# Optimization experiments

Measured on AMD Instinct MI355X. Metric: run time of the kernel, lower is better.

Reference implementation:

```python
import jax, jax.numpy as jnp
import numpy as np

B, S, H, NH = 2, 2048, 1024, 16
HD = H // NH  # 64


def rope_cos_sin(seq_len, dim, base=10000.0, dtype=jnp.float32):
    inv_freq = 1.0 / (base ** (jnp.arange(0, dim, 2, dtype=jnp.float32) / dim))
    t = jnp.arange(seq_len, dtype=jnp.float32)
    freqs = jnp.outer(t, inv_freq)              # [S, dim/2]
    emb = jnp.concatenate([freqs, freqs], -1)   # [S, dim]
    # broadcast shape [1, S, 1, dim]
    return jnp.cos(emb)[None, :, None, :].astype(dtype), jnp.sin(emb)[None, :, None, :].astype(dtype)


def rotate_half(x):
    x1, x2 = x[..., : x.shape[-1] // 2], x[..., x.shape[-1] // 2:]
    return jnp.concatenate([-x2, x1], axis=-1)


def setup_inputs() -> dict:
    key = jax.random.key(0)
    ks = jax.random.split(key, 5)
    sc = 1.0 / np.sqrt(H)
    x = jax.random.normal(ks[0], (B, S, H), jnp.float32)
    Wq = jax.random.normal(ks[1], (H, H), jnp.float32) * sc
    Wk = jax.random.normal(ks[2], (H, H), jnp.float32) * sc
    Wv = jax.random.normal(ks[3], (H, H), jnp.float32) * sc
    Wo = jax.random.normal(ks[4], (H, H), jnp.float32) * sc
    z = jnp.zeros((H,), jnp.float32)
    mask = jnp.tril(jnp.ones((S, S), bool))[None, None]  # causal [1,1,S,S]
    return {"x": x, "Wq": Wq, "bq": z, "Wk": Wk, "bk": z, "Wv": Wv, "bv": z,
            "Wo": Wo, "bo": z, "mask": mask}


def reference(x, Wq, bq, Wk, bk, Wv, bv, Wo, bo, mask):
    b, s, _ = x.shape
    q = (x @ Wq.T + bq).reshape(b, s, NH, HD)
    k = (x @ Wk.T + bk).reshape(b, s, NH, HD)
    v = (x @ Wv.T + bv).reshape(b, s, NH, HD)
    cos, sin = rope_cos_sin(s, HD, dtype=x.dtype)
    q = q * cos + rotate_half(q) * sin
    k = k * cos + rotate_half(k) * sin
    # [b, h, s, s] scores, explicit as in original
    scores = jnp.einsum("bqhd,bkhd->bhqk", q, k) / jnp.sqrt(jnp.asarray(HD, x.dtype))
    scores = jnp.where(mask, scores, jnp.asarray(-jnp.inf, x.dtype))
    attn = jax.nn.softmax(scores, axis=-1)
    out = jnp.einsum("bhqk,bkhd->bqhd", attn, v).reshape(b, s, H)
    return out @ Wo.T + bo
```

## Files before the change

kernel.cpp:

```cpp
#include <hip/hip_runtime.h>

typedef __bf16 bf16;
typedef __bf16 bf16x4 __attribute__((ext_vector_type(4)));
typedef __bf16 bf16x8 __attribute__((ext_vector_type(8)));
typedef float floatx4 __attribute__((ext_vector_type(4)));

#define MFMA16(a, b, c) __builtin_amdgcn_mfma_f32_16x16x32_bf16(a, b, c, 0, 0, 0)

__device__ __forceinline__ void load_lds16(const void* g, void* l) {
    __builtin_amdgcn_global_load_lds(
        (const __attribute__((address_space(1))) unsigned int*)g,
        (__attribute__((address_space(3))) unsigned int*)l, 16, 0, 0);
}

__device__ __forceinline__ bf16x8 scale8(bf16x8 a, float s) {
    bf16x8 o;
    #pragma unroll
    for (int i = 0; i < 8; i++) o[i] = (bf16)((float)a[i] * s);
    return o;
}

__global__ __launch_bounds__(256) void cvt_all_kernel(
    const float* __restrict__ x, const float* __restrict__ wq,
    const float* __restrict__ wk, const float* __restrict__ wv,
    const float* __restrict__ wo,
    bf16* __restrict__ xb, bf16* __restrict__ wqb, bf16* __restrict__ wkb,
    bf16* __restrict__ wvb, bf16* __restrict__ wob)
{
    int bid = blockIdx.x;
    const float* src; bf16* dst; int off;
    if (bid < 4096)      { src = x;  dst = xb;  off = bid; }
    else if (bid < 5120) { src = wq; dst = wqb; off = bid - 4096; }
    else if (bid < 6144) { src = wk; dst = wkb; off = bid - 5120; }
    else if (bid < 7168) { src = wv; dst = wvb; off = bid - 6144; }
    else                 { src = wo; dst = wob; off = bid - 7168; }
    int idx = (off * 256 + threadIdx.x) * 4;
    float4 v = *(const float4*)&src[idx];
    bf16x4 o;
    o[0] = (bf16)v.x; o[1] = (bf16)v.y; o[2] = (bf16)v.z; o[3] = (bf16)v.w;
    *(bf16x4*)&dst[idx] = o;
}

__global__ __launch_bounds__(256) void cvt_kernel(const float* __restrict__ x,
                                                  bf16* __restrict__ xb) {
    int idx = (blockIdx.x * 256 + threadIdx.x) * 4;
    float4 v = *(const float4*)&x[idx];
    bf16x4 o;
    o[0] = (bf16)v.x; o[1] = (bf16)v.y; o[2] = (bf16)v.z; o[3] = (bf16)v.w;
    *(bf16x4*)&xb[idx] = o;
}


#define STAGE_TILES(Asrc, Bsrc, arow, brow)                                   \
    _Pragma("unroll")                                                         \
    for (int t = 0; t < 4; t++) {                                             \
        int R0 = w * 32 + t * 8;                                              \
        int row = R0 + (lane >> 3);                                           \
        int gc = (lane & 7) ^ (row & 7);                                      \
        load_lds16(&Asrc[(size_t)(arow + row) * 1024 + k0 + gc * 8], &As[R0][0]); \
        load_lds16(&Bsrc[(size_t)(brow + row) * 1024 + k0 + gc * 8], &Bs[R0][0]); \
    }

__global__ __launch_bounds__(256) void gemm_qkv_fast(
    const bf16* __restrict__ xb,
    const bf16* __restrict__ Wq, const bf16* __restrict__ Wk,
    const bf16* __restrict__ Wv,
    const float* __restrict__ bq, const float* __restrict__ bk,
    const float* __restrict__ bv,
    bf16* __restrict__ q_ws, bf16* __restrict__ k_ws, bf16* __restrict__ vt_ws)
{
    int m0 = blockIdx.x * 128;
    int n0 = blockIdx.y * 128;
    int sec = n0 >> 10;
    int nw0 = n0 & 1023;
    const bf16* W     = (sec == 0) ? Wq : (sec == 1) ? Wk : Wv;
    const float* bias = (sec == 0) ? bq : (sec == 1) ? bk : bv;

    __shared__ bf16 As[128][64];
    __shared__ bf16 Bs[128][64];

    int tid = threadIdx.x;
    int lane = tid & 63, w = tid >> 6;
    int l15 = lane & 15, quad = lane >> 4;
    int wm = (w >> 1) * 64, wn = (w & 1) * 64;

    floatx4 acc[4][4];
    #pragma unroll
    for (int i = 0; i < 4; i++)
        #pragma unroll
        for (int j = 0; j < 4; j++) acc[i][j] = (floatx4){0.f, 0.f, 0.f, 0.f};

    for (int k0 = 0; k0 < 1024; k0 += 64) {
        __syncthreads();
        STAGE_TILES(xb, W, m0, nw0)
        __syncthreads();
        #pragma unroll
        for (int kk = 0; kk < 2; kk++) {
            int cb = kk * 4 + quad;
            bf16x8 af[4], bfr[4];
            #pragma unroll
            for (int mt = 0; mt < 4; mt++) {
                int row = wm + mt * 16 + l15;
                af[mt] = *(const bf16x8*)&As[row][(cb ^ (row & 7)) * 8];
            }
            #pragma unroll
            for (int nt = 0; nt < 4; nt++) {
                int row = wn + nt * 16 + l15;
                bfr[nt] = *(const bf16x8*)&Bs[row][(cb ^ (row & 7)) * 8];
            }
            #pragma unroll
            for (int mt = 0; mt < 4; mt++)
                #pragma unroll
                for (int nt = 0; nt < 4; nt++)
                    acc[mt][nt] = MFMA16(af[mt], bfr[nt], acc[mt][nt]);
        }
    }

    if (sec < 2) {
        bf16* outp = (sec == 0) ? q_ws : k_ws;
        float inv[2];
        inv[0] = __expf(-(float)l15 * (9.210340371976184f / 32.0f));
        inv[1] = __expf(-(float)(16 + l15) * (9.210340371976184f / 32.0f));
        #pragma unroll
        for (int mt = 0; mt < 4; mt++) {
            #pragma unroll
            for (int r = 0; r < 4; r++) {
                int m = m0 + wm + mt * 16 + quad * 4 + r;
                int bb = m >> 11, s = m & 2047;
                #pragma unroll
                for (int nt = 0; nt < 2; nt++) {
                    int nl1 = nw0 + wn + nt * 16 + l15;
                    int nl2 = nl1 + 32;
                    float x1 = acc[mt][nt][r] + bias[nl1];
                    float x2 = acc[mt][nt + 2][r] + bias[nl2];
                    float ang = (float)s * inv[nt];
                    float sn, cs;
                    __sincosf(ang, &sn, &cs);
                    int hh = nl1 >> 6, d = nl1 & 63;
                    size_t base = ((size_t)(bb * 16 + hh) * 2048 + s) * 64;
                    outp[base + d]      = (bf16)(x1 * cs - x2 * sn);
                    outp[base + d + 32] = (bf16)(x2 * cs + x1 * sn);
                }
            }
        }
    } else {
        #pragma unroll
        for (int mt = 0; mt < 4; mt++) {
            int mbase = m0 + wm + mt * 16 + quad * 4;
            int bb = mbase >> 11, s0 = mbase & 2047;
            #pragma unroll
            for (int nt = 0; nt < 4; nt++) {
                int nl = nw0 + wn + nt * 16 + l15;
                int hh = nl >> 6, d = nl & 63;
                bf16x4 pk;
                #pragma unroll
                for (int r = 0; r < 4; r++) pk[r] = (bf16)(acc[mt][nt][r] + bias[nl]);
                *(bf16x4*)&vt_ws[((size_t)(bb * 16 + hh) * 64 + d) * 2048 + s0] = pk;
            }
        }
    }
}

__global__ __launch_bounds__(256) void gemm_out_fast(
    const bf16* __restrict__ A, const bf16* __restrict__ W,
    const float* __restrict__ bias, float* __restrict__ out)
{
    int m0 = blockIdx.x * 128;
    int n0 = blockIdx.y * 128;

    __shared__ bf16 As[128][64];
    __shared__ bf16 Bs[128][64];

    int tid = threadIdx.x;
    int lane = tid & 63, w = tid >> 6;
    int l15 = lane & 15, quad = lane >> 4;
    int wm = (w >> 1) * 64, wn = (w & 1) * 64;

    floatx4 acc[4][4];
    #pragma unroll
    for (int i = 0; i < 4; i++)
        #pragma unroll
        for (int j = 0; j < 4; j++) acc[i][j] = (floatx4){0.f, 0.f, 0.f, 0.f};

    for (int k0 = 0; k0 < 1024; k0 += 64) {
        __syncthreads();
        STAGE_TILES(A, W, m0, n0)
        __syncthreads();
        #pragma unroll
        for (int kk = 0; kk < 2; kk++) {
            int cb = kk * 4 + quad;
            bf16x8 af[4], bfr[4];
            #pragma unroll
            for (int mt = 0; mt < 4; mt++) {
                int row = wm + mt * 16 + l15;
                af[mt] = *(const bf16x8*)&As[row][(cb ^ (row & 7)) * 8];
            }
            #pragma unroll
            for (int nt = 0; nt < 4; nt++) {
                int row = wn + nt * 16 + l15;
                bfr[nt] = *(const bf16x8*)&Bs[row][(cb ^ (row & 7)) * 8];
            }
            #pragma unroll
            for (int mt = 0; mt < 4; mt++)
                #pragma unroll
                for (int nt = 0; nt < 4; nt++)
                    acc[mt][nt] = MFMA16(af[mt], bfr[nt], acc[mt][nt]);
        }
    }

    #pragma unroll
    for (int mt = 0; mt < 4; mt++) {
        #pragma unroll
        for (int r = 0; r < 4; r++) {
            int m = m0 + wm + mt * 16 + quad * 4 + r;
            #pragma unroll
            for (int nt = 0; nt < 4; nt++) {
                int nl = n0 + wn + nt * 16 + l15;
                out[(size_t)m * 1024 + nl] = acc[mt][nt][r] + bias[nl];
            }
        }
    }
}

__global__ __launch_bounds__(256) void gemm_qkv_f32w(
    const bf16* __restrict__ xb,
    const float* __restrict__ Wq, const float* __restrict__ Wk,
    const float* __restrict__ Wv,
    const float* __restrict__ bq, const float* __restrict__ bk,
    const float* __restrict__ bv,
    bf16* __restrict__ q_ws, bf16* __restrict__ k_ws, bf16* __restrict__ vt_ws)
{
    int m0 = blockIdx.x * 128;
    int n0 = blockIdx.y * 128;
    int sec = n0 >> 10;
    int nw0 = n0 & 1023;
    const float* W    = (sec == 0) ? Wq : (sec == 1) ? Wk : Wv;
    const float* bias = (sec == 0) ? bq : (sec == 1) ? bk : bv;

    __shared__ bf16 As[128][72];
    __shared__ bf16 Bs[128][72];

    int tid = threadIdx.x;
    int lane = tid & 63, w = tid >> 6;
    int l15 = lane & 15, quad = lane >> 4;
    int wm = (w >> 1) * 64, wn = (w & 1) * 64;
    int sr = tid >> 1;
    int sk = (tid & 1) * 32;

    floatx4 acc[4][4];
    #pragma unroll
    for (int i = 0; i < 4; i++)
        #pragma unroll
        for (int j = 0; j < 4; j++) acc[i][j] = (floatx4){0.f, 0.f, 0.f, 0.f};

    for (int k0 = 0; k0 < 1024; k0 += 64) {
        __syncthreads();
        const bf16* ap = &xb[(size_t)(m0 + sr) * 1024 + k0 + sk];
        bf16x8 a0 = *(const bf16x8*)(ap);
        bf16x8 a1 = *(const bf16x8*)(ap + 8);
        bf16x8 a2 = *(const bf16x8*)(ap + 16);
        bf16x8 a3 = *(const bf16x8*)(ap + 24);
        const float* wp = &W[(size_t)(nw0 + sr) * 1024 + k0 + sk];
        bf16x8 bv_[4];
        #pragma unroll
        for (int c = 0; c < 4; c++) {
            float4 f0 = *(const float4*)(wp + c * 8);
            float4 f1 = *(const float4*)(wp + c * 8 + 4);
            bf16x8 t;
            t[0] = (bf16)f0.x; t[1] = (bf16)f0.y; t[2] = (bf16)f0.z; t[3] = (bf16)f0.w;
            t[4] = (bf16)f1.x; t[5] = (bf16)f1.y; t[6] = (bf16)f1.z; t[7] = (bf16)f1.w;
            bv_[c] = t;
        }
        *(bf16x8*)&As[sr][sk + 0]  = a0;
        *(bf16x8*)&As[sr][sk + 8]  = a1;
        *(bf16x8*)&As[sr][sk + 16] = a2;
        *(bf16x8*)&As[sr][sk + 24] = a3;
        #pragma unroll
        for (int c = 0; c < 4; c++) *(bf16x8*)&Bs[sr][sk + c * 8] = bv_[c];
        __syncthreads();
        #pragma unroll
        for (int kk = 0; kk < 64; kk += 32) {
            bf16x8 af[4], bfr[4];
            #pragma unroll
            for (int mt = 0; mt < 4; mt++)
                af[mt] = *(const bf16x8*)&As[wm + mt * 16 + l15][kk + quad * 8];
            #pragma unroll
            for (int nt = 0; nt < 4; nt++)
                bfr[nt] = *(const bf16x8*)&Bs[wn + nt * 16 + l15][kk + quad * 8];
            #pragma unroll
            for (int mt = 0; mt < 4; mt++)
                #pragma unroll
                for (int nt = 0; nt < 4; nt++)
                    acc[mt][nt] = MFMA16(af[mt], bfr[nt], acc[mt][nt]);
        }
    }

    if (sec < 2) {
        bf16* outp = (sec == 0) ? q_ws : k_ws;
        float inv[2];
        inv[0] = __expf(-(float)l15 * (9.210340371976184f / 32.0f));
        inv[1] = __expf(-(float)(16 + l15) * (9.210340371976184f / 32.0f));
        #pragma unroll
        for (int mt = 0; mt < 4; mt++) {
            #pragma unroll
            for (int r = 0; r < 4; r++) {
                int m = m0 + wm + mt * 16 + quad * 4 + r;
                int bb = m >> 11, s = m & 2047;
                #pragma unroll
                for (int nt = 0; nt < 2; nt++) {
                    int nl1 = nw0 + wn + nt * 16 + l15;
                    int nl2 = nl1 + 32;
                    float x1 = acc[mt][nt][r] + bias[nl1];
                    float x2 = acc[mt][nt + 2][r] + bias[nl2];
                    float ang = (float)s * inv[nt];
                    float sn, cs;
                    __sincosf(ang, &sn, &cs);
                    int hh = nl1 >> 6, d = nl1 & 63;
                    size_t base = ((size_t)(bb * 16 + hh) * 2048 + s) * 64;
                    outp[base + d]      = (bf16)(x1 * cs - x2 * sn);
                    outp[base + d + 32] = (bf16)(x2 * cs + x1 * sn);
                }
            }
        }
    } else {
        #pragma unroll
        for (int mt = 0; mt < 4; mt++) {
            int mbase = m0 + wm + mt * 16 + quad * 4;
            int bb = mbase >> 11, s0 = mbase & 2047;
            #pragma unroll
            for (int nt = 0; nt < 4; nt++) {
                int nl = nw0 + wn + nt * 16 + l15;
                int hh = nl >> 6, d = nl & 63;
                bf16x4 pk;
                #pragma unroll
                for (int r = 0; r < 4; r++) pk[r] = (bf16)(acc[mt][nt][r] + bias[nl]);
                *(bf16x4*)&vt_ws[((size_t)(bb * 16 + hh) * 64 + d) * 2048 + s0] = pk;
            }
        }
    }
}

__global__ __launch_bounds__(256) void gemm_out_f32w(
    const bf16* __restrict__ A, const float* __restrict__ W,
    const float* __restrict__ bias, float* __restrict__ out)
{
    int m0 = blockIdx.x * 128;
    int n0 = blockIdx.y * 128;

    __shared__ bf16 As[128][72];
    __shared__ bf16 Bs[128][72];

    int tid = threadIdx.x;
    int lane = tid & 63, w = tid >> 6;
    int l15 = lane & 15, quad = lane >> 4;
    int wm = (w >> 1) * 64, wn = (w & 1) * 64;
    int sr = tid >> 1;
    int sk = (tid & 1) * 32;

    floatx4 acc[4][4];
    #pragma unroll
    for (int i = 0; i < 4; i++)
        #pragma unroll
        for (int j = 0; j < 4; j++) acc[i][j] = (floatx4){0.f, 0.f, 0.f, 0.f};

    for (int k0 = 0; k0 < 1024; k0 += 64) {
        __syncthreads();
        const bf16* ap = &A[(size_t)(m0 + sr) * 1024 + k0 + sk];
        bf16x8 a0 = *(const bf16x8*)(ap);
        bf16x8 a1 = *(const bf16x8*)(ap + 8);
        bf16x8 a2 = *(const bf16x8*)(ap + 16);
        bf16x8 a3 = *(const bf16x8*)(ap + 24);
        const float* wp = &W[(size_t)(n0 + sr) * 1024 + k0 + sk];
        bf16x8 bv_[4];
        #pragma unroll
        for (int c = 0; c < 4; c++) {
            float4 f0 = *(const float4*)(wp + c * 8);
            float4 f1 = *(const float4*)(wp + c * 8 + 4);
            bf16x8 t;
            t[0] = (bf16)f0.x; t[1] = (bf16)f0.y; t[2] = (bf16)f0.z; t[3] = (bf16)f0.w;
            t[4] = (bf16)f1.x; t[5] = (bf16)f1.y; t[6] = (bf16)f1.z; t[7] = (bf16)f1.w;
            bv_[c] = t;
        }
        *(bf16x8*)&As[sr][sk + 0]  = a0;
        *(bf16x8*)&As[sr][sk + 8]  = a1;
        *(bf16x8*)&As[sr][sk + 16] = a2;
        *(bf16x8*)&As[sr][sk + 24] = a3;
        #pragma unroll
        for (int c = 0; c < 4; c++) *(bf16x8*)&Bs[sr][sk + c * 8] = bv_[c];
        __syncthreads();
        #pragma unroll
        for (int kk = 0; kk < 64; kk += 32) {
            bf16x8 af[4], bfr[4];
            #pragma unroll
            for (int mt = 0; mt < 4; mt++)
                af[mt] = *(const bf16x8*)&As[wm + mt * 16 + l15][kk + quad * 8];
            #pragma unroll
            for (int nt = 0; nt < 4; nt++)
                bfr[nt] = *(const bf16x8*)&Bs[wn + nt * 16 + l15][kk + quad * 8];
            #pragma unroll
            for (int mt = 0; mt < 4; mt++)
                #pragma unroll
                for (int nt = 0; nt < 4; nt++)
                    acc[mt][nt] = MFMA16(af[mt], bfr[nt], acc[mt][nt]);
        }
    }

    #pragma unroll
    for (int mt = 0; mt < 4; mt++) {
        #pragma unroll
        for (int r = 0; r < 4; r++) {
            int m = m0 + wm + mt * 16 + quad * 4 + r;
            #pragma unroll
            for (int nt = 0; nt < 4; nt++) {
                int nl = n0 + wn + nt * 16 + l15;
                out[(size_t)m * 1024 + nl] = acc[mt][nt][r] + bias[nl];
            }
        }
    }
}

__global__ __launch_bounds__(512, 4) void attn_kernel(
    const bf16* __restrict__ q_ws, const bf16* __restrict__ k_ws,
    const bf16* __restrict__ vt_ws, bf16* __restrict__ o_ws)
{
    __shared__ bf16 Ks[2][64][64];
    __shared__ bf16 Vt[2][64][64];
    __shared__ bf16 Ps[8][16][72];

    int tid = threadIdx.x;
    int w = tid >> 6, lane = tid & 63;
    int l15 = lane & 15, quad = lane >> 4;

    int bid = blockIdx.x;
    int g = bid & 31;
    int xx = bid >> 5;
    int qt = (xx < 8) ? xx : 23 - xx;
    if (g & 1) qt = 15 - qt;
    int bb = g >> 4, h = g & 15;
    const bf16* qp = q_ws + (size_t)g * 2048 * 64;
    const bf16* kp = k_ws + (size_t)g * 2048 * 64;
    const bf16* vp = vt_ws + (size_t)g * 64 * 2048;
    int qrow = qt * 128 + w * 16;

    int r = w * 8 + (lane >> 3);
    int c = (lane & 7) ^ (r & 7);
    int od = w * 512;

    const float SCL = 0.125f * 1.4426950408889634f;
    const float MFIX = 20.0f;

    bf16x8 qf0 = scale8(*(const bf16x8*)&qp[(size_t)(qrow + l15) * 64 + quad * 8], SCL);
    bf16x8 qf1 = scale8(*(const bf16x8*)&qp[(size_t)(qrow + l15) * 64 + 32 + quad * 8], SCL);

    float l_lane = 0.f;
    floatx4 acc[4];
    #pragma unroll
    for (int nt = 0; nt < 4; nt++) acc[nt] = (floatx4){0.f, 0.f, 0.f, 0.f};

    int nkt = 2 * qt + 2;

    load_lds16(&kp[(size_t)r * 64 + c * 8], &Ks[0][0][0] + od);
    load_lds16(&vp[(size_t)r * 2048 + c * 8], &Vt[0][0][0] + od);

    for (int kt = 0; kt < nkt; kt++) {
        int buf = kt & 1;
        __syncthreads();

        if (kt + 1 < nkt) {
            int kn0 = (kt + 1) * 64;
            load_lds16(&kp[(size_t)(kn0 + r) * 64 + c * 8], &Ks[buf ^ 1][0][0] + od);
            load_lds16(&vp[(size_t)r * 2048 + kn0 + c * 8], &Vt[buf ^ 1][0][0] + od);
        }

        int kt0 = kt * 64;

        floatx4 st[4];
        #pragma unroll
        for (int kb = 0; kb < 4; kb++) {
            int row = kb * 16 + l15;
            int rx = row & 7;
            bf16x8 a0 = *(const bf16x8*)&Ks[buf][row][(quad ^ rx) * 8];
            bf16x8 a1 = *(const bf16x8*)&Ks[buf][row][((quad + 4) ^ rx) * 8];
            floatx4 z = {-MFIX, -MFIX, -MFIX, -MFIX};
            z = MFMA16(a0, qf0, z);
            z = MFMA16(a1, qf1, z);
            st[kb] = z;
        }
        if (kt0 + 63 > qrow) {
            int q = qrow + l15;
            #pragma unroll
            for (int kb = 0; kb < 4; kb++)
                #pragma unroll
                for (int rr = 0; rr < 4; rr++) {
                    int key = kt0 + kb * 16 + quad * 4 + rr;
                    if (key > q) st[kb][rr] = -1e30f;
                }
        }

        #pragma unroll
        for (int kb = 0; kb < 4; kb++) {
            bf16x4 pk;
            #pragma unroll
            for (int rr = 0; rr < 4; rr++) {
                float pv = exp2f(st[kb][rr]);
                l_lane += pv;
                pk[rr] = (bf16)pv;
            }
            *(bf16x4*)&Ps[w][l15][kb * 16 + quad * 4] = pk;
        }

        bf16x8 pb0 = *(const bf16x8*)&Ps[w][l15][quad * 8];
        bf16x8 pb1 = *(const bf16x8*)&Ps[w][l15][32 + quad * 8];
        #pragma unroll
        for (int nt = 0; nt < 4; nt++) {
            int row = nt * 16 + l15;
            int rx = row & 7;
            bf16x8 v0 = *(const bf16x8*)&Vt[buf][row][(quad ^ rx) * 8];
            bf16x8 v1 = *(const bf16x8*)&Vt[buf][row][((quad + 4) ^ rx) * 8];
            acc[nt] = MFMA16(v0, pb0, acc[nt]);
            acc[nt] = MFMA16(v1, pb1, acc[nt]);
        }
    }

    l_lane += __shfl_xor(l_lane, 16, 64);
    l_lane += __shfl_xor(l_lane, 32, 64);
    float inv = 1.f / l_lane;
    int s = qrow + l15;
    #pragma unroll
    for (int nt = 0; nt < 4; nt++) {
        bf16x4 pk;
        #pragma unroll
        for (int rr = 0; rr < 4; rr++) pk[rr] = (bf16)(acc[nt][rr] * inv);
        *(bf16x4*)&o_ws[((size_t)(bb * 2048 + s)) * 1024 + h * 64 + nt * 16 + quad * 4] = pk;
    }
}

extern "C" void kernel_launch(void* const* d_in, const int* in_sizes, int n_in,
                              void* d_out, int out_size, void* d_ws, size_t ws_size,
                              hipStream_t stream) {
    const float* x  = (const float*)d_in[0];
    const float* Wq = (const float*)d_in[1];
    const float* bq = (const float*)d_in[2];
    const float* Wk = (const float*)d_in[3];
    const float* bk = (const float*)d_in[4];
    const float* Wv = (const float*)d_in[5];
    const float* bv = (const float*)d_in[6];
    const float* Wo = (const float*)d_in[7];
    const float* bo = (const float*)d_in[8];
    float* out = (float*)d_out;

    const size_t NELEM = (size_t)2 * 2048 * 1024;
    const size_t WELEM = (size_t)1024 * 1024;
    bf16* xb    = (bf16*)d_ws;
    bf16* q_ws  = xb + NELEM;
    bf16* k_ws  = q_ws + NELEM;
    bf16* vt_ws = k_ws + NELEM;
    bf16* o_ws  = xb;
    bf16* wqb   = vt_ws + NELEM;
    bf16* wkb   = wqb + WELEM;
    bf16* wvb   = wkb + WELEM;
    bf16* wob   = wvb + WELEM;

    bool fast = ws_size >= (size_t)40 * 1024 * 1024;

    if (fast) {
        cvt_all_kernel<<<8192, 256, 0, stream>>>(x, Wq, Wk, Wv, Wo,
                                                 xb, wqb, wkb, wvb, wob);
        gemm_qkv_fast<<<dim3(32, 24), 256, 0, stream>>>(
            xb, wqb, wkb, wvb, bq, bk, bv, q_ws, k_ws, vt_ws);
        attn_kernel<<<512, 512, 0, stream>>>(q_ws, k_ws, vt_ws, o_ws);
        gemm_out_fast<<<dim3(32, 8), 256, 0, stream>>>(o_ws, wob, bo, out);
    } else {
        cvt_kernel<<<4096, 256, 0, stream>>>(x, xb);
        gemm_qkv_f32w<<<dim3(32, 24), 256, 0, stream>>>(
            xb, Wq, Wk, Wv, bq, bk, bv, q_ws, k_ws, vt_ws);
        attn_kernel<<<512, 512, 0, stream>>>(q_ws, k_ws, vt_ws, o_ws);
        gemm_out_f32w<<<dim3(32, 8), 256, 0, stream>>>(o_ws, Wo, bo, out);
    }
}
```

Baseline: 209.6 us.

## Double-buffer LDS tiles in QKV and output GEMMs with single barrier per step

Both projection GEMMs now use two LDS buffers with a K-step of 32 instead of one buffer with a K-step of 64. The next tile's global-to-LDS loads are issued right after a single barrier, so they overlap the MFMA work on the current buffer, and the second barrier per iteration goes away. The XOR swizzle is adapted to the narrower 32-element rows. The trade-off is twice as many loop iterations with fewer MFMAs each, and correctness depends on the barrier also waiting for the outstanding async LDS loads.

```diff
diff --git a/kernel.cpp b/kernel.cpp
--- a/kernel.cpp
+++ b/kernel.cpp
@@ -51,14 +51,50 @@
 }
 
 
-#define STAGE_TILES(Asrc, Bsrc, arow, brow)                                   \
-    _Pragma("unroll")                                                         \
-    for (int t = 0; t < 4; t++) {                                             \
-        int R0 = w * 32 + t * 8;                                              \
-        int row = R0 + (lane >> 3);                                           \
-        int gc = (lane & 7) ^ (row & 7);                                      \
-        load_lds16(&Asrc[(size_t)(arow + row) * 1024 + k0 + gc * 8], &As[R0][0]); \
-        load_lds16(&Bsrc[(size_t)(brow + row) * 1024 + k0 + gc * 8], &Bs[R0][0]); \
+#define PREP_STAGE()                                                          \
+    int u0 = w * 128 + lane;                                                  \
+    int u1 = u0 + 64;                                                         \
+    int r0_ = u0 >> 2, c0_ = ((u0 & 3) ^ ((r0_ >> 1) & 3)) * 8;               \
+    int r1_ = u1 >> 2, c1_ = ((u1 & 3) ^ ((r1_ >> 1) & 3)) * 8;               \
+    int du0 = w * 1024;                                                       \
+    int du1 = du0 + 512;
+
+#define STAGE_PF(Asrc, Bsrc, arow, brow, sbuf, kk0)                           \
+    do {                                                                      \
+        load_lds16(&Asrc[(size_t)((arow) + r0_) * 1024 + (kk0) + c0_],        \
+                   &As[sbuf][0][0] + du0);                                    \
+        load_lds16(&Asrc[(size_t)((arow) + r1_) * 1024 + (kk0) + c1_],        \
+                   &As[sbuf][0][0] + du1);                                    \
+        load_lds16(&Bsrc[(size_t)((brow) + r0_) * 1024 + (kk0) + c0_],        \
+                   &Bs[sbuf][0][0] + du0);                                    \
+        load_lds16(&Bsrc[(size_t)((brow) + r1_) * 1024 + (kk0) + c1_],        \
+                   &Bs[sbuf][0][0] + du1);                                    \
+    } while (0)
+
+#define GEMM_CORE(Asrc, Bsrc, arow, brow)                                     \
+    PREP_STAGE()                                                              \
+    STAGE_PF(Asrc, Bsrc, arow, brow, 0, 0);                                   \
+    _Pragma("unroll 2")                                                       \
+    for (int s = 0; s < 32; s++) {                                            \
+        int sb = s & 1;                                                       \
+        __syncthreads();                                                      \
+        if (s + 1 < 32) STAGE_PF(Asrc, Bsrc, arow, brow, sb ^ 1, (s + 1) * 32); \
+        bf16x8 af[4], bfr[4];                                                 \
+        _Pragma("unroll")                                                     \
+        for (int mt = 0; mt < 4; mt++) {                                      \
+            int row = wm + mt * 16 + l15;                                     \
+            af[mt] = *(const bf16x8*)&As[sb][row][(quad ^ ((row >> 1) & 3)) * 8]; \
+        }                                                                     \
+        _Pragma("unroll")                                                     \
+        for (int nt = 0; nt < 4; nt++) {                                      \
+            int row = wn + nt * 16 + l15;                                     \
+            bfr[nt] = *(const bf16x8*)&Bs[sb][row][(quad ^ ((row >> 1) & 3)) * 8]; \
+        }                                                                     \
+        _Pragma("unroll")                                                     \
+        for (int mt = 0; mt < 4; mt++)                                        \
+            _Pragma("unroll")                                                 \
+            for (int nt = 0; nt < 4; nt++)                                    \
+                acc[mt][nt] = MFMA16(af[mt], bfr[nt], acc[mt][nt]);           \
     }
 
 __global__ __launch_bounds__(256) void gemm_qkv_fast(
@@ -76,8 +112,8 @@
     const bf16* W     = (sec == 0) ? Wq : (sec == 1) ? Wk : Wv;
     const float* bias = (sec == 0) ? bq : (sec == 1) ? bk : bv;
 
-    __shared__ bf16 As[128][64];
-    __shared__ bf16 Bs[128][64];
+    __shared__ bf16 As[2][128][32];
+    __shared__ bf16 Bs[2][128][32];
 
     int tid = threadIdx.x;
     int lane = tid & 63, w = tid >> 6;
@@ -90,31 +126,7 @@
         #pragma unroll
         for (int j = 0; j < 4; j++) acc[i][j] = (floatx4){0.f, 0.f, 0.f, 0.f};
 
-    for (int k0 = 0; k0 < 1024; k0 += 64) {
-        __syncthreads();
-        STAGE_TILES(xb, W, m0, nw0)
-        __syncthreads();
-        #pragma unroll
-        for (int kk = 0; kk < 2; kk++) {
-            int cb = kk * 4 + quad;
-            bf16x8 af[4], bfr[4];
-            #pragma unroll
-            for (int mt = 0; mt < 4; mt++) {
-                int row = wm + mt * 16 + l15;
-                af[mt] = *(const bf16x8*)&As[row][(cb ^ (row & 7)) * 8];
-            }
-            #pragma unroll
-            for (int nt = 0; nt < 4; nt++) {
-                int row = wn + nt * 16 + l15;
-                bfr[nt] = *(const bf16x8*)&Bs[row][(cb ^ (row & 7)) * 8];
-            }
-            #pragma unroll
-            for (int mt = 0; mt < 4; mt++)
-                #pragma unroll
-                for (int nt = 0; nt < 4; nt++)
-                    acc[mt][nt] = MFMA16(af[mt], bfr[nt], acc[mt][nt]);
-        }
-    }
+    GEMM_CORE(xb, W, m0, nw0)
 
     if (sec < 2) {
         bf16* outp = (sec == 0) ? q_ws : k_ws;
@@ -168,8 +180,8 @@
     int m0 = blockIdx.x * 128;
     int n0 = blockIdx.y * 128;
 
-    __shared__ bf16 As[128][64];
-    __shared__ bf16 Bs[128][64];
+    __shared__ bf16 As[2][128][32];
+    __shared__ bf16 Bs[2][128][32];
 
     int tid = threadIdx.x;
     int lane = tid & 63, w = tid >> 6;
@@ -182,31 +194,7 @@
         #pragma unroll
         for (int j = 0; j < 4; j++) acc[i][j] = (floatx4){0.f, 0.f, 0.f, 0.f};
 
-    for (int k0 = 0; k0 < 1024; k0 += 64) {
-        __syncthreads();
-        STAGE_TILES(A, W, m0, n0)
-        __syncthreads();
-        #pragma unroll
-        for (int kk = 0; kk < 2; kk++) {
-            int cb = kk * 4 + quad;
-            bf16x8 af[4], bfr[4];
-            #pragma unroll
-            for (int mt = 0; mt < 4; mt++) {
-                int row = wm + mt * 16 + l15;
-                af[mt] = *(const bf16x8*)&As[row][(cb ^ (row & 7)) * 8];
-            }
-            #pragma unroll
-            for (int nt = 0; nt < 4; nt++) {
-                int row = wn + nt * 16 + l15;
-                bfr[nt] = *(const bf16x8*)&Bs[row][(cb ^ (row & 7)) * 8];
-            }
-            #pragma unroll
-            for (int mt = 0; mt < 4; mt++)
-                #pragma unroll
-                for (int nt = 0; nt < 4; nt++)
-                    acc[mt][nt] = MFMA16(af[mt], bfr[nt], acc[mt][nt]);
-        }
-    }
+    GEMM_CORE(A, W, m0, n0)
 
     #pragma unroll
     for (int mt = 0; mt < 4; mt++) {
```

Result: slower. 215.2 us (+2.7%).
